# Kernel optimization log

Hardware: AMD Instinct MI355X
Metric: run time of the kernel (lower is better)

## Reference

```python
import jax, jax.numpy as jnp
import numpy as np

B, N, ND = 32, 512, 8        # batch, graph_size, node_dim
L, H, D = 4, 8, 512          # layers, heads, embed_dim
DK = D // H                  # key_dim = val_dim = 64
F = 2048                     # feed_forward_hidden
EPS = 1e-5


def setup_inputs() -> dict:
    key = jax.random.key(0)
    ks = jax.random.split(key, 16)
    u = lambda k, shape, s: jax.random.uniform(k, shape, jnp.float32, -s, s)
    x = jax.random.normal(ks[0], (B, N, ND), dtype=jnp.float32)
    mask = jax.random.randint(ks[1], (B, N, N), 0, 2).astype(jnp.int32)  # 1 = masked
    return {
        "x": x,
        "mask": mask,
        # init_embed Linear(node_dim, embed_dim)
        "We": u(ks[2], (ND, D), 1.0 / np.sqrt(ND)),
        "be": u(ks[3], (D,), 1.0 / np.sqrt(ND)),
        # per-head projections, stacked over layers; torch init: uniform(-1/sqrt(last_dim), ...)
        "Wq": u(ks[4], (L, H, D, DK), 1.0 / np.sqrt(DK)),
        "Wk": u(ks[5], (L, H, D, DK), 1.0 / np.sqrt(DK)),
        "Wv": u(ks[6], (L, H, D, DK), 1.0 / np.sqrt(DK)),
        "Wo": u(ks[7], (L, H, DK, D), 1.0 / np.sqrt(D)),
        # BatchNorm1d affine params (torch default: weight=1, bias=0)
        "g1": jnp.ones((L, D), jnp.float32), "bt1": jnp.zeros((L, D), jnp.float32),
        "g2": jnp.ones((L, D), jnp.float32), "bt2": jnp.zeros((L, D), jnp.float32),
        # FFN
        "W1": u(ks[8], (L, D, F), 1.0 / np.sqrt(D)),
        "bf1": u(ks[9], (L, F), 1.0 / np.sqrt(D)),
        "W2": u(ks[10], (L, F, D), 1.0 / np.sqrt(F)),
        "bf2": u(ks[11], (L, D), 1.0 / np.sqrt(F)),
    }


def _batch_norm(h, g, b):
    # BatchNorm1d in training mode over flattened (B*N, D), biased variance
    hf = h.reshape(-1, h.shape[-1])
    mu = hf.mean(axis=0)
    var = hf.var(axis=0)
    return (h - mu) * jax.lax.rsqrt(var + EPS) * g + b


def reference(x, mask, We, be, Wq, Wk, Wv, Wo, g1, bt1, W1, bf1, W2, bf2, g2, bt2):
    m = mask.astype(bool)[None]                      # [1,B,N,N], True = masked
    scale = 1.0 / np.sqrt(Wq.shape[-1])
    h = x @ We + be                                  # [B,N,D]
    for l in range(Wq.shape[0]):
        # hand-rolled per-head MHA (q = h, self-attention)
        Q = jnp.einsum('bnd,hdk->hbnk', h, Wq[l])
        K = jnp.einsum('bnd,hdk->hbnk', h, Wk[l])
        V = jnp.einsum('bnd,hdv->hbnv', h, Wv[l])
        scores = jnp.einsum('hbqk,hbnk->hbqn', Q, K) * scale   # [H,B,N,N]
        scores = jnp.where(m, -jnp.inf, scores)
        attn = jax.nn.softmax(scores, axis=-1)
        attn = jnp.where(m, 0.0, attn)               # second mask-zeroing pass
        heads = jnp.einsum('hbqn,hbnv->hbqv', attn, V)
        out = jnp.einsum('hbqv,hvd->bqd', heads, Wo[l])
        h = _batch_norm(h + out, g1[l], bt1[l])      # residual + BN
        ff = jax.nn.relu(h @ W1[l] + bf1[l]) @ W2[l] + bf2[l]
        h = _batch_norm(h + ff, g2[l], bt2[l])       # residual + BN
    return (h, h.mean(axis=1))
```

## Files before the change

kernel.cpp:

```cpp
#include <hip/hip_runtime.h>
#include <hip/hip_fp16.h>
#include <math.h>

#define BN_ROWS 16384
#define DIM 512
#define FF 2048
#define LAYERS 4
#define NSEQ 512
#define BATCH 32

typedef _Float16 f16;
typedef __attribute__((ext_vector_type(8))) _Float16 f16x8;
typedef __attribute__((ext_vector_type(4))) _Float16 f16x4;
typedef __attribute__((ext_vector_type(4))) float f32x4;
typedef __attribute__((ext_vector_type(16))) float f32x16;
typedef unsigned long long u64;

__device__ __forceinline__ f32x4 mfma_f16(f16x8 a, f16x8 b, f32x4 c) {
    return __builtin_amdgcn_mfma_f32_16x16x32_f16(a, b, c, 0, 0, 0);
}
__device__ __forceinline__ f32x16 mfma32(f16x8 a, f16x8 b, f32x16 c) {
    return __builtin_amdgcn_mfma_f32_32x32x16_f16(a, b, c, 0, 0, 0);
}
__device__ __forceinline__ unsigned pk2u(float x, float y) {
    auto t = __builtin_amdgcn_cvt_pkrtz(x, y);
    return *reinterpret_cast<unsigned*>(&t);
}
__device__ __forceinline__ void gload_lds16(const f16* g, f16* l) {
    __builtin_amdgcn_global_load_lds(
        (const __attribute__((address_space(1))) unsigned int*)g,
        (__attribute__((address_space(3))) unsigned int*)l, 16, 0, 0);
}

__global__ __launch_bounds__(256)
void pack_qkv(const float* __restrict__ Wq, const float* __restrict__ Wk,
              const float* __restrict__ Wv, f16* __restrict__ oh) {
    size_t i = (size_t)blockIdx.x * 256 + threadIdx.x;
    int d = i & 511;
    size_t rr = i >> 9;
    int row = (int)(rr % 1536);
    int lay = (int)(rr / 1536);
    int which = row >> 9, hh = (row >> 6) & 7, k = row & 63;
    const float* W = which == 0 ? Wq : which == 1 ? Wk : Wv;
    oh[i] = (f16)W[(((size_t)lay * 8 + hh) * 512 + d) * 64 + k];
}

__global__ __launch_bounds__(256)
void transpose_w(const float* __restrict__ in, f16* __restrict__ oh, int R, int C) {
    size_t i = (size_t)blockIdx.x * 256 + threadIdx.x;
    int r = (int)(i % R);
    size_t t = i / R;
    int c = (int)(t % C);
    int lay = (int)(t / C);
    oh[i] = (f16)in[((size_t)lay * R + r) * C + c];
}

__global__ __launch_bounds__(256)
void pack_mask(const int* __restrict__ mask, u64* __restrict__ pm) {
    int wid = (blockIdx.x * 256 + threadIdx.x) >> 6;
    int lane = threadIdx.x & 63;
    for (int i = 0; i < 64; i++) {
        size_t word = (size_t)wid * 64 + i;
        u64 bal = __ballot(mask[word * 64 + lane] != 0);
        if (lane == 0) pm[word] = bal;
    }
}

__global__ __launch_bounds__(512)
void embed_kernel(const float* __restrict__ x, const float* __restrict__ We,
                  const float* __restrict__ be, f16* __restrict__ h16) {
    int row = blockIdx.x, d = threadIdx.x;
    const float* xr = x + (size_t)row * 8;
    float acc = be[d];
#pragma unroll
    for (int c = 0; c < 8; c++) acc += xr[c] * We[c * DIM + d];
    h16[(size_t)row * DIM + d] = (f16)acc;
}

template<int OUT>
__global__ __launch_bounds__(512, 6)
void gemm_f16(const f16* __restrict__ A, const f16* __restrict__ Bt,
              const float* __restrict__ bias,
              void* __restrict__ O0, void* __restrict__ O1, void* __restrict__ O2,
              int M, int N, int K) {
    __shared__ f16 As[3][4096];
    __shared__ f16 Bs[3][4096];
    const int gx = gridDim.x;
    const int nwg = gx * gridDim.y;
    const int id = blockIdx.y * gx + blockIdx.x;
    const int chunk = nwg >> 3;
    const int sid = (id & 7) * chunk + (id >> 3);
    const int row0 = (sid / gx) * 128, col0 = (sid % gx) * 128;

    const int tid = threadIdx.x, l = tid & 63, w = tid >> 6;
    const int wr = w & 1, wc = w >> 1;
    const int fr = l & 15, fq = l >> 4;
    const int srow = tid >> 2;
    const int skg = ((tid & 3) ^ ((tid >> 3) & 3)) * 8;
    const int fqs8 = (fq ^ ((fr >> 1) & 3)) * 8;

    f32x4 acc[4][2] = {};
    const f16* Ab = A + (size_t)(row0 + srow) * K + skg;
    const f16* Bb = Bt + (size_t)(col0 + srow) * K + skg;
    const int nt = K >> 5;

    auto stage = [&](int buf, int k0) {
        gload_lds16(Ab + k0, &As[buf][w * 512]);
        gload_lds16(Bb + k0, &Bs[buf][w * 512]);
    };

    stage(0, 0);
    stage(1, 32);

    for (int kt = 0; kt < nt; kt++) {
        const int buf = kt % 3;
        if (kt + 1 < nt) asm volatile("s_waitcnt vmcnt(2)" ::: "memory");
        else             asm volatile("s_waitcnt vmcnt(0)" ::: "memory");
        __builtin_amdgcn_s_barrier();
        __builtin_amdgcn_sched_barrier(0);
        if (kt + 2 < nt) stage((kt + 2) % 3, (kt + 2) * 32);
        f16x8 a[4], b[2];
#pragma unroll
        for (int i = 0; i < 4; i++)
            a[i] = *(const f16x8*)&As[buf][(wr * 64 + i * 16 + fr) * 32 + fqs8];
#pragma unroll
        for (int j = 0; j < 2; j++)
            b[j] = *(const f16x8*)&Bs[buf][(wc * 32 + j * 16 + fr) * 32 + fqs8];
#pragma unroll
        for (int i = 0; i < 4; i++)
#pragma unroll
            for (int j = 0; j < 2; j++)
                acc[i][j] = mfma_f16(a[i], b[j], acc[i][j]);
    }

    if (OUT == 1) {
        f16* C = (f16*)O0;
#pragma unroll
        for (int j = 0; j < 2; j++) {
            int gcol = col0 + wc * 32 + j * 16 + fr;
            float bv = bias[gcol];
#pragma unroll
            for (int i = 0; i < 4; i++) {
                int gr = row0 + wr * 64 + i * 16 + fq * 4;
#pragma unroll
                for (int r = 0; r < 4; r++)
                    C[(size_t)(gr + r) * N + gcol] = (f16)fmaxf(acc[i][j][r] + bv, 0.f);
            }
        }
    } else if (OUT == 2) {
        const float SCQ = 0.18033688011112042f;
        f16* Qo = (f16*)O0; f16* Ko = (f16*)O1; f16* Vo = (f16*)O2;
#pragma unroll
        for (int j = 0; j < 2; j++) {
            int gcol = col0 + wc * 32 + j * 16 + fr;
            if (gcol < 1024) {
                bool isQ = gcol < 512;
                f16* dst = isQ ? Qo : Ko;
                float sc = isQ ? SCQ : 1.0f;
                int cc = gcol & 511;
#pragma unroll
                for (int i = 0; i < 4; i++) {
                    int gr = row0 + wr * 64 + i * 16 + fq * 4;
#pragma unroll
                    for (int r = 0; r < 4; r++)
                        dst[(size_t)(gr + r) * 512 + cc] = (f16)(acc[i][j][r] * sc);
                }
            } else {
                int hh = (gcol - 1024) >> 6, v = gcol & 63;
#pragma unroll
                for (int i = 0; i < 4; i++) {
                    int gr = row0 + wr * 64 + i * 16 + fq * 4;
                    int b = gr >> 9, n = gr & 511;
                    f16x4 sv;
#pragma unroll
                    for (int r = 0; r < 4; r++) sv[r] = (f16)acc[i][j][r];
                    *(f16x4*)&Vo[(((size_t)b * 8 + hh) * 64 + v) * 512 + n] = sv;
                }
            }
        }
    } else {
        f16* hres = (f16*)O0;
        float* st  = (float*)O1;
#pragma unroll
        for (int j = 0; j < 2; j++) {
            int gcol = col0 + wc * 32 + j * 16 + fr;
            float bv = bias ? bias[gcol] : 0.f;
            float csum = 0.f, csq = 0.f;
#pragma unroll
            for (int i = 0; i < 4; i++) {
                int gr = row0 + wr * 64 + i * 16 + fq * 4;
#pragma unroll
                for (int r = 0; r < 4; r++) {
                    size_t idx = (size_t)(gr + r) * N + gcol;
                    float v = acc[i][j][r] + bv + (float)hres[idx];
                    hres[idx] = (f16)v;
                    csum += v; csq += v * v;
                }
            }
            csum += __shfl_down(csum, 32, 64); csum += __shfl_down(csum, 16, 64);
            csq  += __shfl_down(csq,  32, 64); csq  += __shfl_down(csq,  16, 64);
            if (fq == 0) {
                atomicAdd(&st[gcol], csum);
                atomicAdd(&st[gcol + 512], csq);
            }
        }
    }
}

__global__ __launch_bounds__(512, 4)
void attn_flash(const f16* __restrict__ Q, const f16* __restrict__ Kg,
                const f16* __restrict__ Vt, const u64* __restrict__ pmask,
                f16* __restrict__ attf) {
    int id = blockIdx.x;
    int wgid = (id & 7) * 64 + (id >> 3);
    int qc = wgid & 1;
    int gid = wgid >> 1;
    int b = gid & 31, hd = gid >> 5;

    __shared__ f16 Kl[2][4096];
    __shared__ f16 Vl[2][4096];

    const int tid = threadIdx.x, w = tid >> 6, l = tid & 63;
    const int q = l & 31, hi = l >> 5;

    const int brow = qc * 256 + w * 32;
    const size_t qrow = ((size_t)b * NSEQ + brow + q) * DIM + hd * 64;
    f16x8 qb[4];
#pragma unroll
    for (int c16 = 0; c16 < 4; c16++)
        qb[c16] = *(const f16x8*)(Q + qrow + c16 * 16 + hi * 8);

    const f16* ksrc = Kg + (size_t)b * NSEQ * DIM + hd * 64;
    const f16* vsrc = Vt + ((size_t)b * 8 + hd) * 64 * 512;
    const u64* mrowq = pmask + ((size_t)b * NSEQ + brow + q) * 8;

    const int srw = tid & 63, scg = tid >> 6;

    const float THR = 11.0f;
    float mu = -1e30f;
    f32x16 O0 = {}, O1 = {}, S1 = {};

    f16x8 vones;
#pragma unroll
    for (int i = 0; i < 8; i++) vones[i] = (f16)1.0f;

    gload_lds16(ksrc + (size_t)srw * DIM + scg * 8, &Kl[0][tid * 8]);
    gload_lds16(vsrc + (size_t)srw * 512 + scg * 8, &Vl[0][tid * 8]);

    u64 bits = mrowq[0];

    for (int c = 0; c < 8; c++) {
        const int buf = c & 1;
        __syncthreads();
        if (c < 7) {
            const int n1 = (c + 1) * 64;
            gload_lds16(ksrc + (size_t)(n1 + srw) * DIM + scg * 8, &Kl[buf ^ 1][tid * 8]);
            gload_lds16(vsrc + (size_t)srw * 512 + n1 + scg * 8,   &Vl[buf ^ 1][tid * 8]);
        }

        f32x16 ps0 = {}, ps1 = {};
        __builtin_amdgcn_s_setprio(1);
#pragma unroll
        for (int c16 = 0; c16 < 4; c16++) {
            f16x8 kb0 = *(const f16x8*)&Kl[buf][((c16 * 2 + hi) * 64 + q) * 8];
            f16x8 kb1 = *(const f16x8*)&Kl[buf][((c16 * 2 + hi) * 64 + 32 + q) * 8];
            ps0 = mfma32(kb0, qb[c16], ps0);
            ps1 = mfma32(kb1, qb[c16], ps1);
        }
        __builtin_amdgcn_s_setprio(0);

        unsigned blo = (unsigned)bits, bhi = (unsigned)(bits >> 32);
        if (c < 7) bits = mrowq[c + 1];

        float lm = fmaxf(ps0[0], ps1[0]);
#pragma unroll
        for (int r = 1; r < 16; r++) lm = fmaxf(lm, fmaxf(ps0[r], ps1[r]));
        if (__any(lm > mu + THR)) {
            float other = __shfl_xor(lm, 32, 64);
            float mn = fmaxf(mu, fmaxf(lm, other));
            float sc = exp2f(mu - mn);
            mu = mn;
            S1 *= sc; O0 *= sc; O1 *= sc;
        }

        float p0[16], p1[16];
#pragma unroll
        for (int r = 0; r < 16; r++) {
            int n0 = (r & 3) + 8 * (r >> 2) + 4 * hi;
            float e0 = exp2f(ps0[r] - mu);
            float e1 = exp2f(ps1[r] - mu);
            unsigned k0 = ((blo >> n0) & 1u) - 1u;
            unsigned k1 = ((bhi >> n0) & 1u) - 1u;
            p0[r] = __uint_as_float(__float_as_uint(e0) & k0);
            p1[r] = __uint_as_float(__float_as_uint(e1) & k1);
        }

        f16x8 PA[2][2];
#pragma unroll
        for (int ntile = 0; ntile < 2; ntile++) {
            const float* p = ntile ? p1 : p0;
#pragma unroll
            for (int m = 0; m < 2; m++) {
                unsigned a0 = pk2u(p[m * 8 + 0], p[m * 8 + 1]);
                unsigned b0 = pk2u(p[m * 8 + 4], p[m * 8 + 5]);
                auto s0 = __builtin_amdgcn_permlane32_swap(a0, b0, false, false);
                unsigned a1 = pk2u(p[m * 8 + 2], p[m * 8 + 3]);
                unsigned b1 = pk2u(p[m * 8 + 6], p[m * 8 + 7]);
                auto s1 = __builtin_amdgcn_permlane32_swap(a1, b1, false, false);
                unsigned wbuf[4] = {(unsigned)s0[0], (unsigned)s1[0],
                                    (unsigned)s0[1], (unsigned)s1[1]};
                PA[ntile][m] = *reinterpret_cast<f16x8*>(wbuf);
            }
        }

        __builtin_amdgcn_s_setprio(1);
#pragma unroll
        for (int ntile = 0; ntile < 2; ntile++)
#pragma unroll
            for (int m = 0; m < 2; m++) {
                f16x8 pa = PA[ntile][m];
                S1 = mfma32(vones, pa, S1);
                int cg = ntile * 4 + m * 2 + hi;
                f16x8 v0 = *(const f16x8*)&Vl[buf][(cg * 64 + q) * 8];
                f16x8 v1 = *(const f16x8*)&Vl[buf][(cg * 64 + 32 + q) * 8];
                O0 = mfma32(v0, pa, O0);
                O1 = mfma32(v1, pa, O1);
            }
        __builtin_amdgcn_s_setprio(0);
    }

    float inv = 1.f / S1[0];
    f16* orow = attf + ((size_t)b * NSEQ + brow + q) * DIM + hd * 64;
#pragma unroll
    for (int r = 0; r < 16; r += 2) {
        int v = (r & 3) + 8 * (r >> 2) + 4 * hi;
        unsigned w0 = pk2u(O0[r] * inv, O0[r + 1] * inv);
        *(unsigned*)(orow + v) = w0;
        unsigned w1 = pk2u(O1[r] * inv, O1[r + 1] * inv);
        *(unsigned*)(orow + 32 + v) = w1;
    }
}

__global__ __launch_bounds__(256)
void bn_apply(f16* __restrict__ h16, const float* __restrict__ sums,
              const float* __restrict__ g, const float* __restrict__ bt,
              float* __restrict__ outp) {
    size_t i8 = (size_t)blockIdx.x * 256 + threadIdx.x;
    size_t idx = i8 * 8;
    int c = (int)(idx & (DIM - 1));
    f16x8 hv = *(f16x8*)&h16[idx];
    float o[8];
    const float invn = 1.f / BN_ROWS;
#pragma unroll
    for (int j = 0; j < 8; j++) {
        float mu = sums[c + j] * invn;
        float var = sums[DIM + c + j] * invn - mu * mu;
        o[j] = ((float)hv[j] - mu) * rsqrtf(var + 1e-5f) * g[c + j] + bt[c + j];
    }
    f16x8 s;
#pragma unroll
    for (int j = 0; j < 8; j++) s[j] = (f16)o[j];
    *(f16x8*)&h16[idx] = s;
    if (outp) {
        *(float4*)&outp[idx]     = (float4){o[0], o[1], o[2], o[3]};
        *(float4*)&outp[idx + 4] = (float4){o[4], o[5], o[6], o[7]};
    }
}

__global__ __launch_bounds__(512)
void mean_kernel(const float* __restrict__ src, float* __restrict__ out2) {
    int b = blockIdx.x, seg = blockIdx.y, d = threadIdx.x;
    float acc = 0.f;
    for (int n = seg * 64; n < seg * 64 + 64; n++)
        acc += src[((size_t)b * NSEQ + n) * DIM + d];
    atomicAdd(&out2[b * DIM + d], acc * (1.f / NSEQ));
}

extern "C" void kernel_launch(void* const* d_in, const int* in_sizes, int n_in,
                              void* d_out, int out_size, void* d_ws, size_t ws_size,
                              hipStream_t stream) {
    const float* x   = (const float*)d_in[0];
    const int*   mask= (const int*)d_in[1];
    const float* We  = (const float*)d_in[2];
    const float* be  = (const float*)d_in[3];
    const float* Wq  = (const float*)d_in[4];
    const float* Wk  = (const float*)d_in[5];
    const float* Wv  = (const float*)d_in[6];
    const float* Wo  = (const float*)d_in[7];
    const float* g1  = (const float*)d_in[8];
    const float* bt1 = (const float*)d_in[9];
    const float* g2  = (const float*)d_in[10];
    const float* bt2 = (const float*)d_in[11];
    const float* W1  = (const float*)d_in[12];
    const float* bf1 = (const float*)d_in[13];
    const float* W2  = (const float*)d_in[14];
    const float* bf2 = (const float*)d_in[15];
    float* out = (float*)d_out;

    const size_t MiB = 1ull << 20;
    const size_t M1 = (size_t)BN_ROWS * DIM;
    char* base = (char*)d_ws;
    f16*   h16   = (f16*)base;
    f16*   Qf    = (f16*)(base + 16 * MiB);
    f16*   Kf    = (f16*)(base + 32 * MiB);
    f16*   Vt    = (f16*)(base + 48 * MiB);
    f16*   attf  = (f16*)(base + 64 * MiB);
    f16*   ffh   = (f16*)(base + 16 * MiB);
    float* stats = (float*)(base + 80 * MiB);
    u64*   pmask = (u64*)(base + 80 * MiB + 65536);
    f16*   wqkv  = (f16*)(base + 82 * MiB);
    f16*   wo    = wqkv + (size_t)4 * 1536 * 512;
    f16*   w1t   = wo   + (size_t)4 * 512 * 512;
    f16*   w2t   = w1t  + (size_t)4 * 2048 * 512;

    pack_qkv<<<dim3(4 * 1536 * 512 / 256), dim3(256), 0, stream>>>(Wq, Wk, Wv, wqkv);
    transpose_w<<<dim3(4 * 512 * 512 / 256), dim3(256), 0, stream>>>(Wo, wo, 512, 512);
    transpose_w<<<dim3(4 * 512 * 2048 / 256), dim3(256), 0, stream>>>(W1, w1t, 512, 2048);
    transpose_w<<<dim3(4 * 2048 * 512 / 256), dim3(256), 0, stream>>>(W2, w2t, 2048, 512);
    pack_mask<<<dim3(512), dim3(256), 0, stream>>>(mask, pmask);
    hipMemsetAsync(out + M1, 0, BATCH * DIM * sizeof(float), stream);

    embed_kernel<<<dim3(BN_ROWS), dim3(512), 0, stream>>>(x, We, be, h16);

    for (int l = 0; l < LAYERS; l++) {
        gemm_f16<2><<<dim3(1536 / 128, 128), dim3(512), 0, stream>>>(
            h16, wqkv + (size_t)l * 1536 * 512, nullptr, Qf, Kf, Vt,
            BN_ROWS, 1536, 512);

        attn_flash<<<dim3(512), dim3(512), 0, stream>>>(Qf, Kf, Vt, pmask, attf);

        hipMemsetAsync(stats, 0, 1024 * sizeof(float), stream);
        gemm_f16<3><<<dim3(512 / 128, 128), dim3(512), 0, stream>>>(
            attf, wo + (size_t)l * 512 * 512, nullptr, h16, stats, nullptr,
            BN_ROWS, 512, 512);
        bn_apply<<<dim3(M1 / 2048), dim3(256), 0, stream>>>(
            h16, stats, g1 + l * DIM, bt1 + l * DIM, nullptr);

        hipMemsetAsync(stats, 0, 1024 * sizeof(float), stream);
        gemm_f16<1><<<dim3(FF / 128, BN_ROWS / 128), dim3(512), 0, stream>>>(
            h16, w1t + (size_t)l * FF * DIM, bf1 + (size_t)l * FF,
            ffh, nullptr, nullptr, BN_ROWS, FF, DIM);
        gemm_f16<3><<<dim3(512 / 128, 128), dim3(512), 0, stream>>>(
            ffh, w2t + (size_t)l * DIM * FF, bf2 + (size_t)l * DIM,
            h16, stats, nullptr, BN_ROWS, 512, FF);

        float* outp = (l == LAYERS - 1) ? out : nullptr;
        bn_apply<<<dim3(M1 / 2048), dim3(256), 0, stream>>>(
            h16, stats, g2 + l * DIM, bt2 + l * DIM, outp);
    }

    mean_kernel<<<dim3(BATCH, 8), dim3(512), 0, stream>>>(out, out + M1);
}
```

Baseline: 1.097 ms.

## Add dedicated 64x128-tile GEMM with residual+BN-stats epilogue for N=512 GEMMs

The N=512 GEMMs (attention output projection and FFN down-projection) now use a new kernel with 64x128 tiles instead of 128x128. That doubles the grid to 1024 workgroups, and launch bounds allow 8 waves per SIMD. The new kernel uses a triple-buffered LDS pipeline with direct global-to-LDS loads, XCD-aware block swizzling, and the residual add plus BN statistics epilogue. The aim is better CU occupancy and latency hiding for these narrow GEMMs. The cost is more B-tile reloads and twice as many atomics into the stats buffer.

```diff
diff --git a/kernel.cpp b/kernel.cpp
--- a/kernel.cpp
+++ b/kernel.cpp
@@ -147,7 +147,7 @@
                     C[(size_t)(gr + r) * N + gcol] = (f16)fmaxf(acc[i][j][r] + bv, 0.f);
             }
         }
-    } else if (OUT == 2) {
+    } else {
         const float SCQ = 0.18033688011112042f;
         f16* Qo = (f16*)O0; f16* Ko = (f16*)O1; f16* Vo = (f16*)O2;
 #pragma unroll
@@ -178,31 +178,89 @@
                 }
             }
         }
-    } else {
-        f16* hres = (f16*)O0;
-        float* st  = (float*)O1;
-#pragma unroll
-        for (int j = 0; j < 2; j++) {
-            int gcol = col0 + wc * 32 + j * 16 + fr;
-            float bv = bias ? bias[gcol] : 0.f;
-            float csum = 0.f, csq = 0.f;
-#pragma unroll
-            for (int i = 0; i < 4; i++) {
-                int gr = row0 + wr * 64 + i * 16 + fq * 4;
-#pragma unroll
-                for (int r = 0; r < 4; r++) {
-                    size_t idx = (size_t)(gr + r) * N + gcol;
-                    float v = acc[i][j][r] + bv + (float)hres[idx];
-                    hres[idx] = (f16)v;
-                    csum += v; csq += v * v;
-                }
+    }
+}
+
+__global__ __launch_bounds__(512, 8)
+void gemm_f16_s(const f16* __restrict__ A, const f16* __restrict__ Bt,
+                const float* __restrict__ bias,
+                f16* __restrict__ hres, float* __restrict__ st,
+                int M, int N, int K) {
+    __shared__ f16 As[3][2048];
+    __shared__ f16 Bs[3][4096];
+    const int gx = gridDim.x;
+    const int nwg = gx * gridDim.y;
+    const int id = blockIdx.y * gx + blockIdx.x;
+    const int chunk = nwg >> 3;
+    const int sid = (id & 7) * chunk + (id >> 3);
+    const int row0 = (sid / gx) * 64, col0 = (sid % gx) * 128;
+
+    const int tid = threadIdx.x, l = tid & 63, w = tid >> 6;
+    const int wr = w & 1, wc = w >> 1;
+    const int fr = l & 15, fq = l >> 4;
+    const int sr = tid >> 2;
+    const int skg = ((tid & 3) ^ ((tid >> 3) & 3)) * 8;
+    const int fqs8 = (fq ^ ((fr >> 1) & 3)) * 8;
+
+    f32x4 acc[2][2] = {};
+    const f16* Ab = A + (size_t)(row0 + sr) * K + skg;
+    const f16* Bb = Bt + (size_t)(col0 + sr) * K + skg;
+    const int nt = K >> 5;
+
+    auto stage = [&](int buf, int k0) {
+        if (tid < 256) gload_lds16(Ab + k0, &As[buf][w * 512]);
+        gload_lds16(Bb + k0, &Bs[buf][w * 512]);
+    };
+
+    stage(0, 0);
+    stage(1, 32);
+
+    for (int kt = 0; kt < nt; kt++) {
+        const int buf = kt % 3;
+        if (kt + 1 < nt) {
+            if (w < 4) asm volatile("s_waitcnt vmcnt(2)" ::: "memory");
+            else       asm volatile("s_waitcnt vmcnt(1)" ::: "memory");
+        } else {
+            asm volatile("s_waitcnt vmcnt(0)" ::: "memory");
+        }
+        __builtin_amdgcn_s_barrier();
+        __builtin_amdgcn_sched_barrier(0);
+        if (kt + 2 < nt) stage((kt + 2) % 3, (kt + 2) * 32);
+        f16x8 a[2], b[2];
+#pragma unroll
+        for (int i = 0; i < 2; i++)
+            a[i] = *(const f16x8*)&As[buf][(wr * 32 + i * 16 + fr) * 32 + fqs8];
+#pragma unroll
+        for (int j = 0; j < 2; j++)
+            b[j] = *(const f16x8*)&Bs[buf][(wc * 32 + j * 16 + fr) * 32 + fqs8];
+#pragma unroll
+        for (int i = 0; i < 2; i++)
+#pragma unroll
+            for (int j = 0; j < 2; j++)
+                acc[i][j] = mfma_f16(a[i], b[j], acc[i][j]);
+    }
+
+#pragma unroll
+    for (int j = 0; j < 2; j++) {
+        int gcol = col0 + wc * 32 + j * 16 + fr;
+        float bv = bias ? bias[gcol] : 0.f;
+        float csum = 0.f, csq = 0.f;
+#pragma unroll
+        for (int i = 0; i < 2; i++) {
+            int gr = row0 + wr * 32 + i * 16 + fq * 4;
+#pragma unroll
+            for (int r = 0; r < 4; r++) {
+                size_t idx = (size_t)(gr + r) * N + gcol;
+                float v = acc[i][j][r] + bv + (float)hres[idx];
+                hres[idx] = (f16)v;
+                csum += v; csq += v * v;
             }
-            csum += __shfl_down(csum, 32, 64); csum += __shfl_down(csum, 16, 64);
-            csq  += __shfl_down(csq,  32, 64); csq  += __shfl_down(csq,  16, 64);
-            if (fq == 0) {
-                atomicAdd(&st[gcol], csum);
-                atomicAdd(&st[gcol + 512], csq);
-            }
+        }
+        csum += __shfl_down(csum, 32, 64); csum += __shfl_down(csum, 16, 64);
+        csq  += __shfl_down(csq,  32, 64); csq  += __shfl_down(csq,  16, 64);
+        if (fq == 0) {
+            atomicAdd(&st[gcol], csum);
+            atomicAdd(&st[gcol + 512], csq);
         }
     }
 }
@@ -430,8 +488,8 @@
         attn_flash<<<dim3(512), dim3(512), 0, stream>>>(Qf, Kf, Vt, pmask, attf);
 
         hipMemsetAsync(stats, 0, 1024 * sizeof(float), stream);
-        gemm_f16<3><<<dim3(512 / 128, 128), dim3(512), 0, stream>>>(
-            attf, wo + (size_t)l * 512 * 512, nullptr, h16, stats, nullptr,
+        gemm_f16_s<<<dim3(512 / 128, 256), dim3(512), 0, stream>>>(
+            attf, wo + (size_t)l * 512 * 512, nullptr, h16, stats,
             BN_ROWS, 512, 512);
         bn_apply<<<dim3(M1 / 2048), dim3(256), 0, stream>>>(
             h16, stats, g1 + l * DIM, bt1 + l * DIM, nullptr);
@@ -440,9 +498,9 @@
         gemm_f16<1><<<dim3(FF / 128, BN_ROWS / 128), dim3(512), 0, stream>>>(
             h16, w1t + (size_t)l * FF * DIM, bf1 + (size_t)l * FF,
             ffh, nullptr, nullptr, BN_ROWS, FF, DIM);
-        gemm_f16<3><<<dim3(512 / 128, 128), dim3(512), 0, stream>>>(
-            ffh, w2t + (size_t)l * DIM * FF, bf2 + (size_t)l * DIM,
-            h16, stats, nullptr, BN_ROWS, 512, FF);
+        gemm_f16_s<<<dim3(512 / 128, 256), dim3(512), 0, stream>>>(
+            ffh, w2t + (size_t)l * DIM * FF, bf2 + (size_t)l * DIM, h16, stats,
+            BN_ROWS, 512, FF);
 
         float* outp = (l == LAYERS - 1) ? out : nullptr;
         bn_apply<<<dim3(M1 / 2048), dim3(256), 0, stream>>>(
```

After: 1.159 ms. +5.7%, slower.
